# Performance work log

Measured on AMD Instinct MI355X. Metric: run time of the kernel, lower is better.

Reference implementation:

```python
import jax, jax.numpy as jnp
import numpy as np

D_X = 1024
D_TEXT = 768
FUSION_DIM = D_X + D_TEXT  # 1792
M = 16
K = 2


def setup_inputs() -> dict:
    key = jax.random.key(0)
    k1, k2, k3, k4, k5 = jax.random.split(key, 5)
    B, H, W = 256, 32, 32
    x = jax.random.normal(k1, (B, D_X, H, W), dtype=jnp.float32)
    degraded = jax.random.normal(k2, (B, D_TEXT), dtype=jnp.float32)
    # learned params (random so routing is non-trivial)
    w_fusion = jax.random.normal(k3, (FUSION_DIM, FUSION_DIM), dtype=jnp.float32) * (1.0 / np.sqrt(FUSION_DIM))
    b_fusion = jax.random.normal(k4, (FUSION_DIM,), dtype=jnp.float32) * 0.01
    w_gate = jax.random.normal(k5, (FUSION_DIM, M), dtype=jnp.float32) * 0.02
    return {"x": x, "degraded": degraded, "w_fusion": w_fusion,
            "b_fusion": b_fusion, "w_gate": w_gate}


def reference(x, degraded, w_fusion, b_fusion, w_gate):
    B = x.shape[0]
    # global average pool over H,W -> [B, d_x]
    x_pooled = jnp.mean(x, axis=(2, 3))
    fused = jnp.concatenate([x_pooled, degraded], axis=1)        # [B, d_x+d_text]
    fused = jnp.dot(fused, w_fusion) + b_fusion                  # Linear
    fused = jax.nn.gelu(fused, approximate=False)                # exact GELU (torch default)
    clean_logits = jnp.dot(fused, w_gate)                        # [B, M]
    probs_for_mi = jax.nn.softmax(clean_logits, axis=1)
    # eval path: logits = clean_logits (no noise)
    num_consider = min(K + 1, M)
    top_logits, top_indices = jax.lax.top_k(clean_logits, num_consider)
    top_k_logits = top_logits[:, :K]
    top_k_indices = top_indices[:, :K]
    top_k_gates = jax.nn.softmax(top_k_logits, axis=1)
    rows = jnp.arange(B)[:, None]
    gates = jnp.zeros_like(clean_logits).at[rows, top_k_indices].set(top_k_gates)
    moe_loss = jnp.float32(0.0)
    return gates, moe_loss, probs_for_mi, top_k_indices
```

## Files before the change

kernel.cpp:

```cpp
#include <hip/hip_runtime.h>
#include <math.h>

#define D_X      1024
#define D_TEXT   768
#define FDIM     1792
#define BATCH    256
#define M_EXP    16
#define HW_TOT   1024

#define OUT_GATES 0
#define OUT_LOSS  4096
#define OUT_PROBS 4097
#define OUT_IDX   8193

#define NBLK_DEG    224
#define POOL_BLOCKS 2048
#define GRID1       (NBLK_DEG + POOL_BLOCKS)
#define NROWS       (BATCH * D_X)

__global__ __launch_bounds__(256) void pool_deggemm_kernel(const float* __restrict__ x,
                                                           const float* __restrict__ deg,
                                                           const float* __restrict__ W,
                                                           float* __restrict__ fused,
                                                           float* __restrict__ pact2) {
    __shared__ float As1[32][33];
    __shared__ float Ws1[32][64];

    const int bid = blockIdx.x;
    const int tid = threadIdx.x;

    if (bid >= NBLK_DEG) {
        const int pb   = bid - NBLK_DEG;
        const int lane = tid & 63;
        const int gw   = pb * 4 + (tid >> 6);

        for (int r2 = gw * 2; r2 < NROWS; r2 += 2 * 4 * POOL_BLOCKS) {
            const float4* x0 = reinterpret_cast<const float4*>(x + (size_t)r2 * HW_TOT);
            float4 v0[4], v1[4];
#pragma unroll
            for (int k = 0; k < 4; ++k) v0[k] = x0[k * 64 + lane];
#pragma unroll
            for (int k = 0; k < 4; ++k) v1[k] = x0[256 + k * 64 + lane];
            float s0 = 0.0f, s1 = 0.0f;
#pragma unroll
            for (int k = 0; k < 4; ++k) {
                s0 += v0[k].x + v0[k].y + v0[k].z + v0[k].w;
                s1 += v1[k].x + v1[k].y + v1[k].z + v1[k].w;
            }
#pragma unroll
            for (int off = 32; off > 0; off >>= 1) {
                s0 += __shfl_xor(s0, off, 64);
                s1 += __shfl_xor(s1, off, 64);
            }
            if (lane == 0) {
                float2 st;
                st.x = s0 * (1.0f / 1024.0f);
                st.y = s1 * (1.0f / 1024.0f);
                *reinterpret_cast<float2*>(&fused[r2]) = st;
            }
        }
        return;
    }

    const int mb = bid / 28;
    const int nb = bid % 28;
    const int m0 = mb * 32;
    const int n0 = nb * 64;

    const int tx = tid & 15;
    const int ty = tid >> 4;

    const int ar  = tid >> 3;
    const int ak4 = (tid & 7) * 4;
    const int wk  = tid >> 4;
    const int wc4 = (tid & 15) * 4;

    float acc[2][4] = {};

    for (int k0 = 0; k0 < D_TEXT; k0 += 32) {
        __syncthreads();
        {
            const float4 a = *reinterpret_cast<const float4*>(
                deg + (size_t)(m0 + ar) * D_TEXT + k0 + ak4);
            As1[ak4 + 0][ar] = a.x; As1[ak4 + 1][ar] = a.y;
            As1[ak4 + 2][ar] = a.z; As1[ak4 + 3][ar] = a.w;
            *reinterpret_cast<float4*>(&Ws1[wk][wc4]) =
                *reinterpret_cast<const float4*>(W + (size_t)(D_X + k0 + wk) * FDIM + n0 + wc4);
            *reinterpret_cast<float4*>(&Ws1[wk + 16][wc4]) =
                *reinterpret_cast<const float4*>(W + (size_t)(D_X + k0 + wk + 16) * FDIM + n0 + wc4);
        }
        __syncthreads();
#pragma unroll
        for (int kk = 0; kk < 32; ++kk) {
            const float2 a = *reinterpret_cast<const float2*>(&As1[kk][ty * 2]);
            const float4 w = *reinterpret_cast<const float4*>(&Ws1[kk][tx * 4]);
            acc[0][0] = fmaf(a.x, w.x, acc[0][0]);
            acc[0][1] = fmaf(a.x, w.y, acc[0][1]);
            acc[0][2] = fmaf(a.x, w.z, acc[0][2]);
            acc[0][3] = fmaf(a.x, w.w, acc[0][3]);
            acc[1][0] = fmaf(a.y, w.x, acc[1][0]);
            acc[1][1] = fmaf(a.y, w.y, acc[1][1]);
            acc[1][2] = fmaf(a.y, w.z, acc[1][2]);
            acc[1][3] = fmaf(a.y, w.w, acc[1][3]);
        }
    }

#pragma unroll
    for (int i = 0; i < 2; ++i) {
        float4 v;
        v.x = acc[i][0]; v.y = acc[i][1]; v.z = acc[i][2]; v.w = acc[i][3];
        *reinterpret_cast<float4*>(pact2 + (size_t)(m0 + ty * 2 + i) * FDIM + n0 + tx * 4) = v;
    }
}

#define BM 32
#define BN 64
#define BK 64
#define KDIM D_X
#define NITER (KDIM / BK)

#define LOADA(k0)                                                                     \
    pa0 = *reinterpret_cast<const float4*>(A + (size_t)(m0 + ar) * KDIM + (k0) + ak4);       \
    pa1 = *reinterpret_cast<const float4*>(A + (size_t)(m0 + ar + 16) * KDIM + (k0) + ak4);

#define LOADW(k0)                                                                     \
    pw0 = *reinterpret_cast<const float4*>(W + (size_t)((k0) + wr0) * FDIM + n0 + wc4);      \
    pw1 = *reinterpret_cast<const float4*>(W + (size_t)((k0) + wr0 + 16) * FDIM + n0 + wc4); \
    pw2 = *reinterpret_cast<const float4*>(W + (size_t)((k0) + wr0 + 32) * FDIM + n0 + wc4); \
    pw3 = *reinterpret_cast<const float4*>(W + (size_t)((k0) + wr0 + 48) * FDIM + n0 + wc4);

#define STOREA(buf)                                                                   \
    As[buf][ak4 + 0][ar] = pa0.x; As[buf][ak4 + 1][ar] = pa0.y;                       \
    As[buf][ak4 + 2][ar] = pa0.z; As[buf][ak4 + 3][ar] = pa0.w;                       \
    As[buf][ak4 + 0][ar + 16] = pa1.x; As[buf][ak4 + 1][ar + 16] = pa1.y;             \
    As[buf][ak4 + 2][ar + 16] = pa1.z; As[buf][ak4 + 3][ar + 16] = pa1.w;

#define STOREW(buf)                                                                   \
    *reinterpret_cast<float4*>(&Ws[buf][wr0][wc4])      = pw0;                        \
    *reinterpret_cast<float4*>(&Ws[buf][wr0 + 16][wc4]) = pw1;                        \
    *reinterpret_cast<float4*>(&Ws[buf][wr0 + 32][wc4]) = pw2;                        \
    *reinterpret_cast<float4*>(&Ws[buf][wr0 + 48][wc4]) = pw3;

__global__ __launch_bounds__(256) void gemm_gate_kernel(const float* __restrict__ A,
                                                        const float* __restrict__ W,
                                                        const float* __restrict__ pact2,
                                                        const float* __restrict__ bias,
                                                        const float* __restrict__ wg,
                                                        float* __restrict__ part) {
    __shared__ float As[2][BK][BM + 1];
    __shared__ float Ws[2][BK][BN];
    __shared__ float wgs[BN][M_EXP];
    __shared__ float actS[BM][BN + 1];

    const int tid = threadIdx.x;
    const int tx = tid & 15;
    const int ty = tid >> 4;
    const int m0 = blockIdx.x * BM;
    const int n0 = blockIdx.y * BN;

    {
        const int r  = tid >> 2;
        const int c4 = (tid & 3) * 4;
        *reinterpret_cast<float4*>(&wgs[r][c4]) =
            *reinterpret_cast<const float4*>(wg + (size_t)(n0 + r) * M_EXP + c4);
    }

    const int ar  = tid >> 4;
    const int ak4 = (tid & 15) * 4;
    const int wr0 = tid >> 4;
    const int wc4 = (tid & 15) * 4;

    float4 pa0, pa1, pw0, pw1, pw2, pw3;

    LOADA(0); LOADW(0);
    STOREA(0); STOREW(0);
    LOADA(BK); LOADW(BK);

    float acc[2][4];
    {
        const float4 i0 = *reinterpret_cast<const float4*>(
            pact2 + (size_t)(m0 + ty * 2) * FDIM + n0 + tx * 4);
        const float4 i1 = *reinterpret_cast<const float4*>(
            pact2 + (size_t)(m0 + ty * 2 + 1) * FDIM + n0 + tx * 4);
        acc[0][0] = i0.x; acc[0][1] = i0.y; acc[0][2] = i0.z; acc[0][3] = i0.w;
        acc[1][0] = i1.x; acc[1][1] = i1.y; acc[1][2] = i1.z; acc[1][3] = i1.w;
    }
    __syncthreads();

    int cur = 0;
    for (int t = 0; t < NITER; ++t) {
#pragma unroll
        for (int kk = 0; kk < BK; ++kk) {
            const float2 a = *reinterpret_cast<const float2*>(&As[cur][kk][ty * 2]);
            const float4 w = *reinterpret_cast<const float4*>(&Ws[cur][kk][tx * 4]);
            acc[0][0] = fmaf(a.x, w.x, acc[0][0]);
            acc[0][1] = fmaf(a.x, w.y, acc[0][1]);
            acc[0][2] = fmaf(a.x, w.z, acc[0][2]);
            acc[0][3] = fmaf(a.x, w.w, acc[0][3]);
            acc[1][0] = fmaf(a.y, w.x, acc[1][0]);
            acc[1][1] = fmaf(a.y, w.y, acc[1][1]);
            acc[1][2] = fmaf(a.y, w.z, acc[1][2]);
            acc[1][3] = fmaf(a.y, w.w, acc[1][3]);
        }
        if (t < NITER - 1) {
            const int nxt = cur ^ 1;
            STOREA(nxt); STOREW(nxt);
            if (t < NITER - 2) {
                const int k0 = (t + 2) * BK;
                LOADA(k0); LOADW(k0);
            }
            __syncthreads();
            cur = nxt;
        }
    }

#pragma unroll
    for (int i = 0; i < 2; ++i) {
        const int m = ty * 2 + i;
#pragma unroll
        for (int j = 0; j < 4; ++j) {
            const int n = tx * 4 + j;
            const float v = acc[i][j] + bias[n0 + n];
            actS[m][n] = v * 0.5f * (1.0f + erff(v * 0.70710678118654752440f));
        }
    }
    __syncthreads();

    const int pm = tid >> 3;
    const int pe = (tid & 7) * 2;
    float s0 = 0.0f, s1 = 0.0f;
#pragma unroll
    for (int n = 0; n < BN; ++n) {
        const float a = actS[pm][n];
        s0 = fmaf(a, wgs[n][pe], s0);
        s1 = fmaf(a, wgs[n][pe + 1], s1);
    }
    float* pr = part + ((size_t)blockIdx.y * BATCH + m0 + pm) * M_EXP + pe;
    pr[0] = s0;
    pr[1] = s1;
}

#define NNB (FDIM / BN)

__global__ __launch_bounds__(64) void finalize_kernel(const float* __restrict__ part,
                                                      float* __restrict__ out) {
    const int b = blockIdx.x * 64 + threadIdx.x;

    float l[M_EXP];
#pragma unroll
    for (int m = 0; m < M_EXP; ++m) l[m] = 0.0f;

    for (int nb = 0; nb < NNB; ++nb) {
        const float4* pr = reinterpret_cast<const float4*>(part + ((size_t)nb * BATCH + b) * M_EXP);
#pragma unroll
        for (int q = 0; q < 4; ++q) {
            const float4 v = pr[q];
            l[q * 4 + 0] += v.x;
            l[q * 4 + 1] += v.y;
            l[q * 4 + 2] += v.z;
            l[q * 4 + 3] += v.w;
        }
    }

    float mx = l[0];
#pragma unroll
    for (int m = 1; m < M_EXP; ++m) mx = fmaxf(mx, l[m]);
    float e[M_EXP], s = 0.0f;
#pragma unroll
    for (int m = 0; m < M_EXP; ++m) { e[m] = expf(l[m] - mx); s += e[m]; }
    const float inv = 1.0f / s;
#pragma unroll
    for (int m = 0; m < M_EXP; ++m) out[OUT_PROBS + b * M_EXP + m] = e[m] * inv;

    int i0 = 0; float v0 = l[0];
#pragma unroll
    for (int m = 1; m < M_EXP; ++m) if (l[m] > v0) { v0 = l[m]; i0 = m; }
    int i1 = -1; float v1 = -INFINITY;
#pragma unroll
    for (int m = 0; m < M_EXP; ++m) if (m != i0 && l[m] > v1) { v1 = l[m]; i1 = m; }

    const float t = expf(v1 - v0);
    const float g0 = 1.0f / (1.0f + t);
    const float g1 = t * g0;

#pragma unroll
    for (int m = 0; m < M_EXP; ++m) out[OUT_GATES + b * M_EXP + m] = 0.0f;
    out[OUT_GATES + b * M_EXP + i0] = g0;
    out[OUT_GATES + b * M_EXP + i1] = g1;

    out[OUT_IDX + b * 2 + 0] = (float)i0;
    out[OUT_IDX + b * 2 + 1] = (float)i1;

    if (b == 0) out[OUT_LOSS] = 0.0f;
}

extern "C" void kernel_launch(void* const* d_in, const int* in_sizes, int n_in,
                              void* d_out, int out_size, void* d_ws, size_t ws_size,
                              hipStream_t stream) {
    const float* x        = (const float*)d_in[0];
    const float* degraded = (const float*)d_in[1];
    const float* w_fusion = (const float*)d_in[2];
    const float* b_fusion = (const float*)d_in[3];
    const float* w_gate   = (const float*)d_in[4];
    float* out = (float*)d_out;

    float* fused = (float*)d_ws;
    float* pact2 = fused + (size_t)BATCH * D_X;
    float* part  = pact2 + (size_t)BATCH * FDIM;

    pool_deggemm_kernel<<<GRID1, 256, 0, stream>>>(x, degraded, w_fusion, fused, pact2);

    gemm_gate_kernel<<<dim3(BATCH / BM, FDIM / BN), 256, 0, stream>>>(fused, w_fusion, pact2,
                                                                     b_fusion, w_gate, part);

    finalize_kernel<<<BATCH / 64, 64, 0, stream>>>(part, out);
}
```

Before: 258.5 us.

## Fuse pooled-x GEMM into pooling blocks as split-K slices; fold finalize via last-block atomic

```diff
diff --git a/kernel.cpp b/kernel.cpp
--- a/kernel.cpp
+++ b/kernel.cpp
@@ -13,29 +13,35 @@
 #define OUT_PROBS 4097
 #define OUT_IDX   8193
 
-#define NBLK_DEG    224
-#define POOL_BLOCKS 2048
-#define GRID1       (NBLK_DEG + POOL_BLOCKS)
-#define NROWS       (BATCH * D_X)
-
-__global__ __launch_bounds__(256) void pool_deggemm_kernel(const float* __restrict__ x,
-                                                           const float* __restrict__ deg,
-                                                           const float* __restrict__ W,
-                                                           float* __restrict__ fused,
-                                                           float* __restrict__ pact2) {
+#define NBLK_DEG 224
+#define NCH      16
+#define CHW      64
+#define NBLK_PG  (NCH * BATCH)
+#define GRID1    (NBLK_DEG + NBLK_PG)
+
+__global__ __launch_bounds__(256) void pool_gemm_kernel(const float* __restrict__ x,
+                                                        const float* __restrict__ deg,
+                                                        const float* __restrict__ W,
+                                                        float* __restrict__ pslice,
+                                                        float* __restrict__ pact2) {
     __shared__ float As1[32][33];
     __shared__ float Ws1[32][64];
+    __shared__ float vs[CHW];
 
     const int bid = blockIdx.x;
     const int tid = threadIdx.x;
 
     if (bid >= NBLK_DEG) {
-        const int pb   = bid - NBLK_DEG;
-        const int lane = tid & 63;
-        const int gw   = pb * 4 + (tid >> 6);
-
-        for (int r2 = gw * 2; r2 < NROWS; r2 += 2 * 4 * POOL_BLOCKS) {
-            const float4* x0 = reinterpret_cast<const float4*>(x + (size_t)r2 * HW_TOT);
+        const int pb    = bid - NBLK_DEG;
+        const int chunk = pb >> 8;
+        const int b     = pb & 255;
+        const int w     = tid >> 6;
+        const int lane  = tid & 63;
+
+        for (int rp = 0; rp < 8; ++rp) {
+            const int cl = w * 16 + rp * 2;
+            const float4* x0 = reinterpret_cast<const float4*>(
+                x + ((size_t)b * D_X + chunk * CHW + cl) * HW_TOT);
             float4 v0[4], v1[4];
 #pragma unroll
             for (int k = 0; k < 4; ++k) v0[k] = x0[k * 64 + lane];
@@ -53,12 +59,24 @@
                 s1 += __shfl_xor(s1, off, 64);
             }
             if (lane == 0) {
-                float2 st;
-                st.x = s0 * (1.0f / 1024.0f);
-                st.y = s1 * (1.0f / 1024.0f);
-                *reinterpret_cast<float2*>(&fused[r2]) = st;
-            }
-        }
+                vs[cl]     = s0 * (1.0f / 1024.0f);
+                vs[cl + 1] = s1 * (1.0f / 1024.0f);
+            }
+        }
+        __syncthreads();
+
+        float s[7] = {};
+        const float* wb = W + (size_t)(chunk * CHW) * FDIM + tid;
+#pragma unroll 4
+        for (int c = 0; c < CHW; ++c) {
+            const float v = vs[c];
+            const float* wr = wb + (size_t)c * FDIM;
+#pragma unroll
+            for (int j = 0; j < 7; ++j) s[j] = fmaf(v, wr[j * 256], s[j]);
+        }
+        float* po = pslice + ((size_t)chunk * BATCH + b) * FDIM + tid;
+#pragma unroll
+        for (int j = 0; j < 7; ++j) po[j * 256] = s[j];
         return;
     }
 
@@ -115,46 +133,19 @@
 
 #define BM 32
 #define BN 64
-#define BK 64
-#define KDIM D_X
-#define NITER (KDIM / BK)
-
-#define LOADA(k0)                                                                     \
-    pa0 = *reinterpret_cast<const float4*>(A + (size_t)(m0 + ar) * KDIM + (k0) + ak4);       \
-    pa1 = *reinterpret_cast<const float4*>(A + (size_t)(m0 + ar + 16) * KDIM + (k0) + ak4);
-
-#define LOADW(k0)                                                                     \
-    pw0 = *reinterpret_cast<const float4*>(W + (size_t)((k0) + wr0) * FDIM + n0 + wc4);      \
-    pw1 = *reinterpret_cast<const float4*>(W + (size_t)((k0) + wr0 + 16) * FDIM + n0 + wc4); \
-    pw2 = *reinterpret_cast<const float4*>(W + (size_t)((k0) + wr0 + 32) * FDIM + n0 + wc4); \
-    pw3 = *reinterpret_cast<const float4*>(W + (size_t)((k0) + wr0 + 48) * FDIM + n0 + wc4);
-
-#define STOREA(buf)                                                                   \
-    As[buf][ak4 + 0][ar] = pa0.x; As[buf][ak4 + 1][ar] = pa0.y;                       \
-    As[buf][ak4 + 2][ar] = pa0.z; As[buf][ak4 + 3][ar] = pa0.w;                       \
-    As[buf][ak4 + 0][ar + 16] = pa1.x; As[buf][ak4 + 1][ar + 16] = pa1.y;             \
-    As[buf][ak4 + 2][ar + 16] = pa1.z; As[buf][ak4 + 3][ar + 16] = pa1.w;
-
-#define STOREW(buf)                                                                   \
-    *reinterpret_cast<float4*>(&Ws[buf][wr0][wc4])      = pw0;                        \
-    *reinterpret_cast<float4*>(&Ws[buf][wr0 + 16][wc4]) = pw1;                        \
-    *reinterpret_cast<float4*>(&Ws[buf][wr0 + 32][wc4]) = pw2;                        \
-    *reinterpret_cast<float4*>(&Ws[buf][wr0 + 48][wc4]) = pw3;
-
-__global__ __launch_bounds__(256) void gemm_gate_kernel(const float* __restrict__ A,
-                                                        const float* __restrict__ W,
-                                                        const float* __restrict__ pact2,
-                                                        const float* __restrict__ bias,
-                                                        const float* __restrict__ wg,
-                                                        float* __restrict__ part) {
-    __shared__ float As[2][BK][BM + 1];
-    __shared__ float Ws[2][BK][BN];
+
+__global__ __launch_bounds__(256) void reduce_gate_kernel(const float* __restrict__ pslice,
+                                                          const float* __restrict__ pact2,
+                                                          const float* __restrict__ bias,
+                                                          const float* __restrict__ wg,
+                                                          float* __restrict__ part,
+                                                          int* __restrict__ done,
+                                                          float* __restrict__ out) {
+    __shared__ float actS[BM][BN + 1];
     __shared__ float wgs[BN][M_EXP];
-    __shared__ float actS[BM][BN + 1];
+    __shared__ int isLast;
 
     const int tid = threadIdx.x;
-    const int tx = tid & 15;
-    const int ty = tid >> 4;
     const int m0 = blockIdx.x * BM;
     const int n0 = blockIdx.y * BN;
 
@@ -165,65 +156,30 @@
             *reinterpret_cast<const float4*>(wg + (size_t)(n0 + r) * M_EXP + c4);
     }
 
-    const int ar  = tid >> 4;
-    const int ak4 = (tid & 15) * 4;
-    const int wr0 = tid >> 4;
-    const int wc4 = (tid & 15) * 4;
-
-    float4 pa0, pa1, pw0, pw1, pw2, pw3;
-
-    LOADA(0); LOADW(0);
-    STOREA(0); STOREW(0);
-    LOADA(BK); LOADW(BK);
-
-    float acc[2][4];
+    const int m  = tid >> 3;
+    const int n8 = (tid & 7) * 8;
+    const size_t rowoff = (size_t)(m0 + m) * FDIM + n0 + n8;
+
+    float vv[8];
     {
-        const float4 i0 = *reinterpret_cast<const float4*>(
-            pact2 + (size_t)(m0 + ty * 2) * FDIM + n0 + tx * 4);
-        const float4 i1 = *reinterpret_cast<const float4*>(
-            pact2 + (size_t)(m0 + ty * 2 + 1) * FDIM + n0 + tx * 4);
-        acc[0][0] = i0.x; acc[0][1] = i0.y; acc[0][2] = i0.z; acc[0][3] = i0.w;
-        acc[1][0] = i1.x; acc[1][1] = i1.y; acc[1][2] = i1.z; acc[1][3] = i1.w;
-    }
-    __syncthreads();
-
-    int cur = 0;
-    for (int t = 0; t < NITER; ++t) {
-#pragma unroll
-        for (int kk = 0; kk < BK; ++kk) {
-            const float2 a = *reinterpret_cast<const float2*>(&As[cur][kk][ty * 2]);
-            const float4 w = *reinterpret_cast<const float4*>(&Ws[cur][kk][tx * 4]);
-            acc[0][0] = fmaf(a.x, w.x, acc[0][0]);
-            acc[0][1] = fmaf(a.x, w.y, acc[0][1]);
-            acc[0][2] = fmaf(a.x, w.z, acc[0][2]);
-            acc[0][3] = fmaf(a.x, w.w, acc[0][3]);
-            acc[1][0] = fmaf(a.y, w.x, acc[1][0]);
-            acc[1][1] = fmaf(a.y, w.y, acc[1][1]);
-            acc[1][2] = fmaf(a.y, w.z, acc[1][2]);
-            acc[1][3] = fmaf(a.y, w.w, acc[1][3]);
-        }
-        if (t < NITER - 1) {
-            const int nxt = cur ^ 1;
-            STOREA(nxt); STOREW(nxt);
-            if (t < NITER - 2) {
-                const int k0 = (t + 2) * BK;
-                LOADA(k0); LOADW(k0);
-            }
-            __syncthreads();
-            cur = nxt;
-        }
-    }
-
-#pragma unroll
-    for (int i = 0; i < 2; ++i) {
-        const int m = ty * 2 + i;
-#pragma unroll
-        for (int j = 0; j < 4; ++j) {
-            const int n = tx * 4 + j;
-            const float v = acc[i][j] + bias[n0 + n];
-            actS[m][n] = v * 0.5f * (1.0f + erff(v * 0.70710678118654752440f));
-        }
-    }
+        const float4 p0 = *reinterpret_cast<const float4*>(pact2 + rowoff);
+        const float4 p1 = *reinterpret_cast<const float4*>(pact2 + rowoff + 4);
+        const float4 b0 = *reinterpret_cast<const float4*>(bias + n0 + n8);
+        const float4 b1 = *reinterpret_cast<const float4*>(bias + n0 + n8 + 4);
+        vv[0] = p0.x + b0.x; vv[1] = p0.y + b0.y; vv[2] = p0.z + b0.z; vv[3] = p0.w + b0.w;
+        vv[4] = p1.x + b1.x; vv[5] = p1.y + b1.y; vv[6] = p1.z + b1.z; vv[7] = p1.w + b1.w;
+    }
+    for (int ch = 0; ch < NCH; ++ch) {
+        const float4 q0 = *reinterpret_cast<const float4*>(
+            pslice + (size_t)ch * BATCH * FDIM + rowoff);
+        const float4 q1 = *reinterpret_cast<const float4*>(
+            pslice + (size_t)ch * BATCH * FDIM + rowoff + 4);
+        vv[0] += q0.x; vv[1] += q0.y; vv[2] += q0.z; vv[3] += q0.w;
+        vv[4] += q1.x; vv[5] += q1.y; vv[6] += q1.z; vv[7] += q1.w;
+    }
+#pragma unroll
+    for (int j = 0; j < 8; ++j)
+        actS[m][n8 + j] = vv[j] * 0.5f * (1.0f + erff(vv[j] * 0.70710678118654752440f));
     __syncthreads();
 
     const int pm = tid >> 3;
@@ -238,60 +194,62 @@
     float* pr = part + ((size_t)blockIdx.y * BATCH + m0 + pm) * M_EXP + pe;
     pr[0] = s0;
     pr[1] = s1;
-}
-
-#define NNB (FDIM / BN)
-
-__global__ __launch_bounds__(64) void finalize_kernel(const float* __restrict__ part,
-                                                      float* __restrict__ out) {
-    const int b = blockIdx.x * 64 + threadIdx.x;
-
-    float l[M_EXP];
-#pragma unroll
-    for (int m = 0; m < M_EXP; ++m) l[m] = 0.0f;
-
-    for (int nb = 0; nb < NNB; ++nb) {
-        const float4* pr = reinterpret_cast<const float4*>(part + ((size_t)nb * BATCH + b) * M_EXP);
-#pragma unroll
-        for (int q = 0; q < 4; ++q) {
-            const float4 v = pr[q];
-            l[q * 4 + 0] += v.x;
-            l[q * 4 + 1] += v.y;
-            l[q * 4 + 2] += v.z;
-            l[q * 4 + 3] += v.w;
-        }
-    }
-
-    float mx = l[0];
-#pragma unroll
-    for (int m = 1; m < M_EXP; ++m) mx = fmaxf(mx, l[m]);
-    float e[M_EXP], s = 0.0f;
-#pragma unroll
-    for (int m = 0; m < M_EXP; ++m) { e[m] = expf(l[m] - mx); s += e[m]; }
-    const float inv = 1.0f / s;
-#pragma unroll
-    for (int m = 0; m < M_EXP; ++m) out[OUT_PROBS + b * M_EXP + m] = e[m] * inv;
-
-    int i0 = 0; float v0 = l[0];
-#pragma unroll
-    for (int m = 1; m < M_EXP; ++m) if (l[m] > v0) { v0 = l[m]; i0 = m; }
-    int i1 = -1; float v1 = -INFINITY;
-#pragma unroll
-    for (int m = 0; m < M_EXP; ++m) if (m != i0 && l[m] > v1) { v1 = l[m]; i1 = m; }
-
-    const float t = expf(v1 - v0);
-    const float g0 = 1.0f / (1.0f + t);
-    const float g1 = t * g0;
-
-#pragma unroll
-    for (int m = 0; m < M_EXP; ++m) out[OUT_GATES + b * M_EXP + m] = 0.0f;
-    out[OUT_GATES + b * M_EXP + i0] = g0;
-    out[OUT_GATES + b * M_EXP + i1] = g1;
-
-    out[OUT_IDX + b * 2 + 0] = (float)i0;
-    out[OUT_IDX + b * 2 + 1] = (float)i1;
-
-    if (b == 0) out[OUT_LOSS] = 0.0f;
+
+    __threadfence();
+    __syncthreads();
+    if (tid == 0) {
+        const int prev = __hip_atomic_fetch_add(done, 1, __ATOMIC_ACQ_REL,
+                                                __HIP_MEMORY_SCOPE_AGENT);
+        isLast = (prev == 8 * 28 - 1);
+    }
+    __syncthreads();
+    if (!isLast) return;
+
+    {
+        const int b = tid;
+        float l[M_EXP];
+#pragma unroll
+        for (int mm = 0; mm < M_EXP; ++mm) l[mm] = 0.0f;
+        for (int nb2 = 0; nb2 < FDIM / BN; ++nb2) {
+            const float4* prr = reinterpret_cast<const float4*>(
+                part + ((size_t)nb2 * BATCH + b) * M_EXP);
+#pragma unroll
+            for (int q = 0; q < 4; ++q) {
+                const float4 v = prr[q];
+                l[q * 4 + 0] += v.x;
+                l[q * 4 + 1] += v.y;
+                l[q * 4 + 2] += v.z;
+                l[q * 4 + 3] += v.w;
+            }
+        }
+        float mx = l[0];
+#pragma unroll
+        for (int mm = 1; mm < M_EXP; ++mm) mx = fmaxf(mx, l[mm]);
+        float e[M_EXP], s = 0.0f;
+#pragma unroll
+        for (int mm = 0; mm < M_EXP; ++mm) { e[mm] = expf(l[mm] - mx); s += e[mm]; }
+        const float inv = 1.0f / s;
+#pragma unroll
+        for (int mm = 0; mm < M_EXP; ++mm) out[OUT_PROBS + b * M_EXP + mm] = e[mm] * inv;
+
+        int i0 = 0; float v0 = l[0];
+#pragma unroll
+        for (int mm = 1; mm < M_EXP; ++mm) if (l[mm] > v0) { v0 = l[mm]; i0 = mm; }
+        int i1 = -1; float v1 = -INFINITY;
+#pragma unroll
+        for (int mm = 0; mm < M_EXP; ++mm) if (mm != i0 && l[mm] > v1) { v1 = l[mm]; i1 = mm; }
+
+        const float t = expf(v1 - v0);
+        const float g0 = 1.0f / (1.0f + t);
+        const float g1 = t * g0;
+#pragma unroll
+        for (int mm = 0; mm < M_EXP; ++mm) out[OUT_GATES + b * M_EXP + mm] = 0.0f;
+        out[OUT_GATES + b * M_EXP + i0] = g0;
+        out[OUT_GATES + b * M_EXP + i1] = g1;
+        out[OUT_IDX + b * 2 + 0] = (float)i0;
+        out[OUT_IDX + b * 2 + 1] = (float)i1;
+        if (b == 0) out[OUT_LOSS] = 0.0f;
+    }
 }
 
 extern "C" void kernel_launch(void* const* d_in, const int* in_sizes, int n_in,
@@ -304,14 +262,15 @@
     const float* w_gate   = (const float*)d_in[4];
     float* out = (float*)d_out;
 
-    float* fused = (float*)d_ws;
-    float* pact2 = fused + (size_t)BATCH * D_X;
-    float* part  = pact2 + (size_t)BATCH * FDIM;
-
-    pool_deggemm_kernel<<<GRID1, 256, 0, stream>>>(x, degraded, w_fusion, fused, pact2);
-
-    gemm_gate_kernel<<<dim3(BATCH / BM, FDIM / BN), 256, 0, stream>>>(fused, w_fusion, pact2,
-                                                                     b_fusion, w_gate, part);
-
-    finalize_kernel<<<BATCH / 64, 64, 0, stream>>>(part, out);
+    float* pslice = (float*)d_ws;
+    float* pact2  = pslice + (size_t)NCH * BATCH * FDIM;
+    float* part   = pact2 + (size_t)BATCH * FDIM;
+    int*   done   = (int*)(part + (size_t)28 * BATCH * M_EXP);
+
+    hipMemsetAsync(done, 0, sizeof(int), stream);
+
+    pool_gemm_kernel<<<GRID1, 256, 0, stream>>>(x, degraded, w_fusion, pslice, pact2);
+
+    reduce_gate_kernel<<<dim3(BATCH / BM, FDIM / BN), 256, 0, stream>>>(pslice, pact2, b_fusion,
+                                                                       w_gate, part, done, out);
 }
```

Result: slower. 289.8 us (+12.1%).
